# Kernel optimization log

Measured on AMD Instinct MI355X. Metric: run time of the kernel, lower is better.

The kernel has to match this reference:

```python
import jax, jax.numpy as jnp
import numpy as np

FS = 256  # sampling_rate
BANDS = [(0.5, 45.0), (0.5, 4.0), (4.0, 8.0), (8.0, 13.0), (13.0, 30.0), (30.0, 45.0)]
EPS = 1e-8


def _bandpass(sig, lo, hi):
    # FFT-domain brick-wall bandpass, matching bandpass_filter_fft
    T = sig.shape[-1]
    F = jnp.fft.rfft(sig, axis=-1)
    freqs = np.fft.rfftfreq(T, d=1.0 / FS)
    mask = jnp.asarray(((freqs >= lo) & (freqs <= hi)).astype(np.float32))
    return jnp.fft.irfft(F * mask, n=T, axis=-1)


def _phase(sig):
    # Hilbert transform -> instantaneous phase
    T = sig.shape[-1]
    h = np.zeros(T, np.float32)
    if T % 2 == 0:
        h[0] = 1.0; h[T // 2] = 1.0; h[1:T // 2] = 2.0
    else:
        h[0] = 1.0; h[1:(T + 1) // 2] = 2.0
    analytic = jnp.fft.ifft(jnp.fft.fft(sig, axis=-1) * jnp.asarray(h), axis=-1)
    return jnp.angle(analytic)


def _zscore(x):
    # matches torch: (x - mean) / (std_unbiased + 1e-8)
    m = x.mean(-1, keepdims=True)
    s = jnp.std(x, axis=-1, keepdims=True, ddof=1)
    return (x - m) / (s + EPS)


def _band_feats(e1, e2, lo, hi):
    B, C, T = e1.shape
    f1 = _bandpass(e1, lo, hi)
    f2 = _bandpass(e2, lo, hi)
    p1 = f1 ** 2
    p2 = f2 ** 2
    ph1 = _phase(f1)
    ph2 = _phase(f2)

    # PLV = |mean_t exp(i(phi1_i - phi2_j))| -> complex matmul over T
    z1 = jnp.exp(1j * ph1)                       # (B,C,T) complex64
    z2c = jnp.exp(-1j * ph2)
    plv = jnp.abs(jnp.einsum('bit,bjt->bij', z1, z2c)) / T

    # pairwise phase differences (B,C,C,T) -- honors the original full CxC structure
    pd = ph1[:, :, None, :] - ph2[:, None, :, :]
    s = jnp.sign(pd)
    pli = jnp.abs(s.mean(-1))

    # wPLI: power-weighted sign, weights normalized over T per (i,j)
    w = (p1[:, :, None, :] + p2[:, None, :, :]) * 0.5
    wn = w / (w.sum(-1, keepdims=True) + EPS)
    wpli = jnp.abs((s * wn).sum(-1))

    # Coherence: |X_i Y_j*|^2 / (|X_i|^2 |Y_j|^2 + eps), mean over freqs
    X1 = jnp.fft.rfft(f1, axis=-1)
    X2 = jnp.fft.rfft(f2, axis=-1)
    P1 = jnp.abs(X1) ** 2                        # (B,C,F)
    P2 = jnp.abs(X2) ** 2
    pw = P1[:, :, None, :] * P2[:, None, :, :]   # == |pxy|^2 == pxx*pyy
    coh = (pw / (pw + EPS)).mean(-1)

    # Power correlation: z-score over T then matmul / T
    pz1 = _zscore(p1)
    pz2 = _zscore(p2)
    pcorr = jnp.einsum('bit,bjt->bij', pz1, pz2) / T

    # Phase difference magnitude
    phdiff = jnp.abs(pd).mean(-1)

    # Time-domain correlation
    tz1 = _zscore(f1)
    tz2 = _zscore(f2)
    tcorr = jnp.einsum('bit,bjt->bij', tz1, tz2) / T

    # feature order: PLV, PLI, wPLI, Coherence, Power_Corr, Phase_Diff, Time_Corr
    return jnp.stack([plv, pli, wpli, coh, pcorr, phdiff, tcorr], axis=1)  # (B,7,C,C)


def setup_inputs() -> dict:
    key = jax.random.key(0)
    k1, k2 = jax.random.split(key)
    eeg1 = jax.random.normal(k1, (4, 64, 2048), dtype=jnp.float32)
    eeg2 = jax.random.normal(k2, (4, 64, 2048), dtype=jnp.float32)
    return {"eeg1": eeg1, "eeg2": eeg2}


def reference(eeg1, eeg2):
    # feature_type='all' -> all 7 features, 6 bands -> (B, 6, 7, C, C)
    feats = [_band_feats(eeg1, eeg2, lo, hi) for lo, hi in BANDS]
    return jnp.stack(feats, axis=1)
```

## Files before the change

kernel.cpp:

```cpp
#include <hip/hip_runtime.h>
#include <math.h>

__constant__ int c_klo[6] = {4, 4, 32, 64, 104, 240};
__constant__ int c_nk[6]  = {357, 29, 33, 41, 137, 121};

#define PI2_N 0.0030679615757712823f

__global__ __launch_bounds__(256) void k_dft(const float* __restrict__ e1,
                                             const float* __restrict__ e2,
                                             float2* __restrict__ coef,
                                             float* __restrict__ pwr) {
  __shared__ float xs[2048];
  __shared__ float red[4][64][2];
  int sig = blockIdx.x;
  int b = sig >> 7, side = (sig >> 6) & 1, ch = sig & 63;
  int bside = b * 2 + side;
  const float* src = (side ? e2 : e1) + (size_t)(b * 64 + ch) * 2048;
  for (int q = 0; q < 2; ++q) {
    int i4 = q * 256 + threadIdx.x;
    ((float4*)xs)[i4] = ((const float4*)src)[i4];
  }
  __syncthreads();
  int binlane = threadIdx.x & 63, tch = threadIdx.x >> 6;
  int t0 = tch << 9;
  const float* xp = xs + t0;
  for (int rnd = 0; rnd < 6; ++rnd) {
    int kidx = rnd * 64 + binlane;
    int k = kidx + 4;
    float wr, wi, sr, si;
    sincosf(-(float)((k * t0) & 2047) * PI2_N, &wi, &wr);
    sincosf(-(float)k * PI2_N, &si, &sr);
    float are = 0.f, aim = 0.f;
    for (int tt = 0; tt < 512; tt += 4) {
      float4 xv = *(const float4*)(xp + tt);
      float nr, ni;
      are = fmaf(xv.x, wr, are); aim = fmaf(xv.x, wi, aim);
      nr = fmaf(wr, sr, -(wi * si)); ni = fmaf(wr, si, wi * sr); wr = nr; wi = ni;
      are = fmaf(xv.y, wr, are); aim = fmaf(xv.y, wi, aim);
      nr = fmaf(wr, sr, -(wi * si)); ni = fmaf(wr, si, wi * sr); wr = nr; wi = ni;
      are = fmaf(xv.z, wr, are); aim = fmaf(xv.z, wi, aim);
      nr = fmaf(wr, sr, -(wi * si)); ni = fmaf(wr, si, wi * sr); wr = nr; wi = ni;
      are = fmaf(xv.w, wr, are); aim = fmaf(xv.w, wi, aim);
      nr = fmaf(wr, sr, -(wi * si)); ni = fmaf(wr, si, wi * sr); wr = nr; wi = ni;
    }
    red[tch][binlane][0] = are;
    red[tch][binlane][1] = aim;
    __syncthreads();
    if (tch == 0 && kidx < 357) {
      float rr = red[0][binlane][0] + red[1][binlane][0] + red[2][binlane][0] + red[3][binlane][0];
      float ri = red[0][binlane][1] + red[1][binlane][1] + red[2][binlane][1] + red[3][binlane][1];
      int a = (bside * 357 + kidx) * 64 + ch;
      coef[a] = make_float2(rr, ri);
      pwr[a] = rr * rr + ri * ri;
    }
    __syncthreads();
  }
}

__global__ __launch_bounds__(256, 1) void k_analytic(const float2* __restrict__ coef,
                                                     float* __restrict__ fields,
                                                     float* __restrict__ statp4) {
  __shared__ float Fs[65 * 128];
  __shared__ float Ltr[4 * 64 * 65];
  int tchunk = blockIdx.x, bside = blockIdx.y;
  int lane = threadIdx.x & 63;
  int wv = threadIdx.x >> 6;
  int ch0 = wv * 16;
  int t = tchunk * 64 + lane;
  float Rr, Ri;
  sincosf((float)t * PI2_N, &Ri, &Rr);
  float asr[16], asi[16];
#pragma unroll
  for (int c = 0; c < 16; ++c) { asr[c] = 0.f; asi[c] = 0.f; }

  auto emit = [&](int bb, const float (&xr)[16], const float (&xi)[16]) {
#pragma unroll
    for (int c = 0; c < 16; ++c) {
      float re = xr[c] * (1.f / 1024.f);
      float im = xi[c] * (1.f / 1024.f);
      float mag2 = fmaf(re, re, im * im);
      float rinv = mag2 > 0.f ? rsqrtf(mag2) : 0.f;
      float cc = mag2 > 0.f ? re * rinv : 1.f;
      float ss = im * rinv;
      float ph = atan2f(im, re);
      int ca = (ch0 + c) * 65 + lane;
      Ltr[ca] = ph;
      Ltr[4160 + ca] = cc;
      Ltr[8320 + ca] = ss;
      Ltr[12480 + ca] = re;
    }
    __syncthreads();
    size_t pb = (size_t)((bb * 8 + bside) * 4) * 131072 + (size_t)tchunk * 4096;
    for (int f = 0; f < 4; ++f) {
      float* op = fields + pb + (size_t)f * 131072;
      const float* lp = Ltr + f * 4160;
      for (int idx = threadIdx.x; idx < 1024; idx += 256) {
        int tt = idx >> 4;
        int c4 = (idx & 15) * 4;
        float4 v = make_float4(lp[(c4 + 0) * 65 + tt], lp[(c4 + 1) * 65 + tt],
                               lp[(c4 + 2) * 65 + tt], lp[(c4 + 3) * 65 + tt]);
        *(float4*)(op + tt * 64 + c4) = v;
      }
    }
    if (threadIdx.x < 64) {
      const float* lp = Ltr + 12480 + threadIdx.x * 65;
      float s = 0.f;
      for (int tt = 0; tt < 64; ++tt) { float v = lp[tt]; float p = v * v; s = fmaf(p, p, s); }
      statp4[((bb * 8 + bside) * 32 + tchunk) * 64 + threadIdx.x] = s;
    }
    __syncthreads();
  };

  for (int bnd = 1; bnd <= 5; ++bnd) {
    int klo = c_klo[bnd], nk = c_nk[bnd];
    float ar_[16], ai_[16];
#pragma unroll
    for (int c = 0; c < 16; ++c) { ar_[c] = 0.f; ai_[c] = 0.f; }
    float Wr, Wi;
    { int m = (klo * t) & 2047; sincosf((float)m * PI2_N, &Wi, &Wr); }
    for (int c0 = 0; c0 < nk; c0 += 64) {
      int kc = min(64, nk - c0);
      __syncthreads();
      {
        int cbase = (bside * 357 + (klo - 4) + c0) * 64;
        const float4* srcp = (const float4*)(coef + cbase);
        for (int idx = threadIdx.x; idx < kc * 32; idx += 256)
          ((float4*)Fs)[idx] = srcp[idx];
      }
      __syncthreads();
      if (c0 == 0 && bnd >= 2) {
        const float4* Fk = ((const float4*)Fs) + (ch0 >> 1);
#pragma unroll
        for (int q = 0; q < 8; ++q) {
          float4 F = Fk[q];
          asr[2 * q]     = fmaf(-F.x, Wr, asr[2 * q]);     asr[2 * q]     = fmaf( F.y, Wi, asr[2 * q]);
          asi[2 * q]     = fmaf(-F.x, Wi, asi[2 * q]);     asi[2 * q]     = fmaf(-F.y, Wr, asi[2 * q]);
          asr[2 * q + 1] = fmaf(-F.z, Wr, asr[2 * q + 1]); asr[2 * q + 1] = fmaf( F.w, Wi, asr[2 * q + 1]);
          asi[2 * q + 1] = fmaf(-F.z, Wi, asi[2 * q + 1]); asi[2 * q + 1] = fmaf(-F.w, Wr, asi[2 * q + 1]);
        }
      }
      const float4* Fp = ((const float4*)Fs) + (ch0 >> 1);
      float4 Fa[8];
#pragma unroll
      for (int q = 0; q < 8; ++q) Fa[q] = Fp[q];
      for (int kk = 0; kk < kc; ++kk) {
        float4 Fb[8];
        const float4* Fn = Fp + 32;
#pragma unroll
        for (int q = 0; q < 8; ++q) Fb[q] = Fn[q];
#pragma unroll
        for (int q = 0; q < 8; ++q) {
          float4 F = Fa[q];
          ar_[2 * q]     = fmaf(F.x, Wr, ar_[2 * q]);     ar_[2 * q]     = fmaf(-F.y, Wi, ar_[2 * q]);
          ai_[2 * q]     = fmaf(F.x, Wi, ai_[2 * q]);     ai_[2 * q]     = fmaf( F.y, Wr, ai_[2 * q]);
          ar_[2 * q + 1] = fmaf(F.z, Wr, ar_[2 * q + 1]); ar_[2 * q + 1] = fmaf(-F.w, Wi, ar_[2 * q + 1]);
          ai_[2 * q + 1] = fmaf(F.z, Wi, ai_[2 * q + 1]); ai_[2 * q + 1] = fmaf( F.w, Wr, ai_[2 * q + 1]);
        }
        float t0r = Wr * Rr, t1i = Wr * Ri;
        Wr = fmaf(-Wi, Ri, t0r);
        Wi = fmaf(Wi, Rr, t1i);
#pragma unroll
        for (int q = 0; q < 8; ++q) Fa[q] = Fb[q];
        Fp += 32;
      }
    }
#pragma unroll
    for (int c = 0; c < 16; ++c) { asr[c] += ar_[c]; asi[c] += ai_[c]; }
    emit(bnd, ar_, ai_);
  }
  emit(0, asr, asi);
}

__global__ __launch_bounds__(256) void k_statred(const float* __restrict__ statp4,
                                                 const float* __restrict__ pwr,
                                                 float* __restrict__ stats) {
  int gid = blockIdx.x * 256 + threadIdx.x;
  int band = gid >> 9, bsd = (gid >> 6) & 7, ch = gid & 63;
  int klo = c_klo[band], nk = c_nk[band];
  const float* pp = pwr + ((bsd * 357) + (klo - 4)) * 64 + ch;
  float sp = 0.f;
  for (int kk = 0; kk < nk; ++kk) sp += pp[kk * 64];
  sp *= (1.f / 1024.f);
  const float* qp = statp4 + (size_t)((band * 8 + bsd) * 32) * 64 + ch;
  float sq = 0.f;
  for (int tc = 0; tc < 32; ++tc) sq += qp[tc * 64];
  stats[gid * 2] = sp;
  stats[gid * 2 + 1] = sq;
}

__global__ __launch_bounds__(256) void k_pairs(const float* __restrict__ fields,
                                               float* __restrict__ part) {
  __shared__ float li[4 * 16 * 32];
  __shared__ float lj[4 * 16 * 64];
  int ts = blockIdx.x, itile = blockIdx.y, bb = blockIdx.z;
  int band = bb >> 2, b = bb & 3;
  int tid = threadIdx.x;
  int ti = tid >> 4, tj = tid & 15;
  const float* pi = fields + (size_t)((band * 8 + b * 2 + 0) * 4) * 131072;
  const float* pj = fields + (size_t)((band * 8 + b * 2 + 1) * 4) * 131072;
  float aP[2][4], aQ[2][4], aSg[2][4], aS1[2][4], aS2[2][4], aAp[2][4], aPp[2][4], aFf[2][4];
#pragma unroll
  for (int il = 0; il < 2; ++il)
#pragma unroll
    for (int jl = 0; jl < 4; ++jl) {
      aP[il][jl] = 0.f; aQ[il][jl] = 0.f; aSg[il][jl] = 0.f; aS1[il][jl] = 0.f;
      aS2[il][jl] = 0.f; aAp[il][jl] = 0.f; aPp[il][jl] = 0.f; aFf[il][jl] = 0.f;
    }
  int tb = ts * 128;
  for (int sub = 0; sub < 8; ++sub) {
    int t0 = tb + sub * 16;
#pragma unroll
    for (int q = 0; q < 2; ++q) {
      int fl = (q * 256 + tid) * 4;
      int f = fl >> 9, tt = (fl >> 5) & 15, cc = fl & 31;
      *(float4*)&li[fl] = *(const float4*)(pi + (size_t)f * 131072 + (t0 + tt) * 64 + itile * 32 + cc);
    }
#pragma unroll
    for (int q = 0; q < 4; ++q) {
      int fl = (q * 256 + tid) * 4;
      int f = fl >> 10, tt = (fl >> 6) & 15, cc = fl & 63;
      *(float4*)&lj[fl] = *(const float4*)(pj + (size_t)f * 131072 + (t0 + tt) * 64 + cc);
    }
    __syncthreads();
#pragma unroll 2
    for (int tt = 0; tt < 16; ++tt) {
      float2 ph1 = *(const float2*)&li[tt * 32 + ti * 2];
      float2 c1 = *(const float2*)&li[512 + tt * 32 + ti * 2];
      float2 s1 = *(const float2*)&li[1024 + tt * 32 + ti * 2];
      float2 f1 = *(const float2*)&li[1536 + tt * 32 + ti * 2];
      float4 ph2 = *(const float4*)&lj[tt * 64 + tj * 4];
      float4 c2 = *(const float4*)&lj[1024 + tt * 64 + tj * 4];
      float4 s2 = *(const float4*)&lj[2048 + tt * 64 + tj * 4];
      float4 f2 = *(const float4*)&lj[3072 + tt * 64 + tj * 4];
      float ph1a[2] = {ph1.x, ph1.y}, c1a[2] = {c1.x, c1.y}, s1a[2] = {s1.x, s1.y}, f1a[2] = {f1.x, f1.y};
      float ph2a[4] = {ph2.x, ph2.y, ph2.z, ph2.w};
      float c2a[4] = {c2.x, c2.y, c2.z, c2.w};
      float s2a[4] = {s2.x, s2.y, s2.z, s2.w};
      float f2a[4] = {f2.x, f2.y, f2.z, f2.w};
      float p1a[2] = {f1a[0] * f1a[0], f1a[1] * f1a[1]};
      float n1a[2] = {-p1a[0], -p1a[1]};
      float p2a[4] = {f2a[0] * f2a[0], f2a[1] * f2a[1], f2a[2] * f2a[2], f2a[3] * f2a[3]};
      float n2a[4] = {-p2a[0], -p2a[1], -p2a[2], -p2a[3]};
#pragma unroll
      for (int il = 0; il < 2; ++il) {
#pragma unroll
        for (int jl = 0; jl < 4; ++jl) {
          float pd = ph1a[il] - ph2a[jl];
          bool pos = pd > 0.f;
          aSg[il][jl] += pos ? 1.f : -1.f;
          aS1[il][jl] += pos ? p1a[il] : n1a[il];
          aS2[il][jl] += pos ? p2a[jl] : n2a[jl];
          aAp[il][jl] += fabsf(pd);
          aP[il][jl] = fmaf(c1a[il], c2a[jl], aP[il][jl]);
          aP[il][jl] = fmaf(s1a[il], s2a[jl], aP[il][jl]);
          aQ[il][jl] = fmaf(s1a[il], c2a[jl], aQ[il][jl]);
          aQ[il][jl] = fmaf(-c1a[il], s2a[jl], aQ[il][jl]);
          aPp[il][jl] = fmaf(p1a[il], p2a[jl], aPp[il][jl]);
          aFf[il][jl] = fmaf(f1a[il], f2a[jl], aFf[il][jl]);
        }
      }
    }
    __syncthreads();
  }
  int pb = (bb * 16 + ts) * 8;
#pragma unroll
  for (int il = 0; il < 2; ++il) {
    int ro = itile * 2048 + (ti * 2 + il) * 64 + tj * 4;
    *(float4*)&part[(size_t)(pb + 0) * 4096 + ro] = make_float4(aP[il][0], aP[il][1], aP[il][2], aP[il][3]);
    *(float4*)&part[(size_t)(pb + 1) * 4096 + ro] = make_float4(aQ[il][0], aQ[il][1], aQ[il][2], aQ[il][3]);
    *(float4*)&part[(size_t)(pb + 2) * 4096 + ro] = make_float4(aSg[il][0], aSg[il][1], aSg[il][2], aSg[il][3]);
    *(float4*)&part[(size_t)(pb + 3) * 4096 + ro] = make_float4(aS1[il][0], aS1[il][1], aS1[il][2], aS1[il][3]);
    *(float4*)&part[(size_t)(pb + 4) * 4096 + ro] = make_float4(aS2[il][0], aS2[il][1], aS2[il][2], aS2[il][3]);
    *(float4*)&part[(size_t)(pb + 5) * 4096 + ro] = make_float4(aAp[il][0], aAp[il][1], aAp[il][2], aAp[il][3]);
    *(float4*)&part[(size_t)(pb + 6) * 4096 + ro] = make_float4(aPp[il][0], aPp[il][1], aPp[il][2], aPp[il][3]);
    *(float4*)&part[(size_t)(pb + 7) * 4096 + ro] = make_float4(aFf[il][0], aFf[il][1], aFf[il][2], aFf[il][3]);
  }
}

__global__ __launch_bounds__(256) void k_final(const float* __restrict__ part,
                                               const float* __restrict__ stats,
                                               const float* __restrict__ pwr,
                                               float* __restrict__ out) {
  int gid = blockIdx.x * 256 + threadIdx.x;
  int bb = gid >> 12, rem = gid & 4095;
  int band = bb >> 2, b = bb & 3;
  int i = rem >> 6, j = rem & 63;
  float S[8];
#pragma unroll
  for (int a = 0; a < 8; ++a) S[a] = 0.f;
  const float* pp = part + (size_t)bb * 16 * 8 * 4096 + rem;
  for (int ts = 0; ts < 16; ++ts)
#pragma unroll
    for (int a = 0; a < 8; ++a) S[a] += pp[(ts * 8 + a) * 4096];
  const float* st1 = stats + (size_t)((band * 8 + b * 2 + 0) * 64 + i) * 2;
  const float* st2 = stats + (size_t)((band * 8 + b * 2 + 1) * 64 + j) * 2;
  float sp1 = st1[0], sq1 = st1[1];
  float sp2 = st2[0], sq2 = st2[1];
  const float T = 2048.f, Ti = 1.f / 2048.f, Vi = 1.f / 2047.f;
  float plv = sqrtf(S[0] * S[0] + S[1] * S[1]) * Ti;
  float pli = fabsf(S[2]) * Ti;
  float wpli = fabsf(0.5f * (S[3] + S[4])) / (0.5f * (sp1 + sp2) + 1e-8f);
  int kl = c_klo[band] - 4, n = c_nk[band];
  const float* P1 = pwr + ((b * 2 + 0) * 357 + kl) * 64 + i;
  const float* P2 = pwr + ((b * 2 + 1) * 357 + kl) * 64 + j;
  float coh = 0.f;
  for (int kk = 0; kk < n; ++kk) {
    float r = P1[kk * 64] * P2[kk * 64];
    coh += __fdividef(r, r + 1e-8f);
  }
  coh *= (1.f / 1025.f);
  float mp1 = sp1 * Ti, mp2 = sp2 * Ti;
  float sd1 = sqrtf(fmaxf((sq1 - T * mp1 * mp1) * Vi, 0.f));
  float sd2 = sqrtf(fmaxf((sq2 - T * mp2 * mp2) * Vi, 0.f));
  float pcorr = (S[6] - T * mp1 * mp2) / ((sd1 + 1e-8f) * (sd2 + 1e-8f)) * Ti;
  float phd = S[5] * Ti;
  float se1 = sqrtf(sp1 * Vi);
  float se2 = sqrtf(sp2 * Vi);
  float tcorr = S[7] / ((se1 + 1e-8f) * (se2 + 1e-8f)) * Ti;
  size_t ob = (size_t)((b * 6 + band) * 7) * 4096 + rem;
  out[ob] = plv;
  out[ob + 4096] = pli;
  out[ob + 2 * 4096] = wpli;
  out[ob + 3 * 4096] = coh;
  out[ob + 4 * 4096] = pcorr;
  out[ob + 5 * 4096] = phd;
  out[ob + 6 * 4096] = tcorr;
}

extern "C" void kernel_launch(void* const* d_in, const int* in_sizes, int n_in,
                              void* d_out, int out_size, void* d_ws, size_t ws_size,
                              hipStream_t stream) {
  const float* e1 = (const float*)d_in[0];
  const float* e2 = (const float*)d_in[1];
  float* out = (float*)d_out;
  char* ws = (char*)d_ws;
  size_t off = 0;
  auto alloc = [&](size_t bytes) -> void* {
    void* p = ws + off;
    off += (bytes + 255) & ~(size_t)255;
    return p;
  };
  float2* coef = (float2*)alloc((size_t)8 * 357 * 64 * 8);
  float* pwr = (float*)alloc((size_t)8 * 357 * 64 * 4);
  float* fields = (float*)alloc((size_t)6 * 8 * 4 * 2048 * 64 * 4);
  float* statp4 = (float*)alloc((size_t)6 * 8 * 32 * 64 * 4);
  float* stats = (float*)alloc((size_t)6 * 8 * 64 * 2 * 4);
  float* part = (float*)alloc((size_t)24 * 16 * 8 * 4096 * 4);
  (void)in_sizes; (void)n_in; (void)out_size; (void)ws_size;

  hipLaunchKernelGGL(k_dft, dim3(512), dim3(256), 0, stream, e1, e2, coef, pwr);
  hipLaunchKernelGGL(k_analytic, dim3(32, 8), dim3(256), 0, stream, coef, fields, statp4);
  hipLaunchKernelGGL(k_statred, dim3(12), dim3(256), 0, stream, statp4, pwr, stats);
  hipLaunchKernelGGL(k_pairs, dim3(16, 2, 24), dim3(256), 0, stream, fields, part);
  hipLaunchKernelGGL(k_final, dim3(384), dim3(256), 0, stream, part, stats, pwr, out);
}
```

Baseline: 401.8 us.

## Split analytic-signal synthesis across band groups and move phase math into pair kernel

The analytic-signal kernel now runs on three independent frequency splits (bands 1-3, band 4, band 5) per block instead of one serial walk over all bands. It reads coefficients straight from global memory and stores only the real and imaginary parts. A new kernel builds band 0 by summing bands 1-5 and removing the overlapping boundary bins. The pair kernel now computes phase, cos and sin on load, uses full 64x64 tiles with 4x4 register blocking, and accumulates the fourth-power statistics. Time correlation is taken from a Parseval dot product over the DFT coefficients in the final kernel, which drops one accumulator. The aim is more parallelism in the serial synthesis stage and less field memory traffic, at the cost of redundant atan2 work and higher register pressure in the pair kernel.

```diff
diff --git a/kernel.cpp b/kernel.cpp
--- a/kernel.cpp
+++ b/kernel.cpp
@@ -57,241 +57,247 @@
   }
 }
 
-__global__ __launch_bounds__(256, 1) void k_analytic(const float2* __restrict__ coef,
-                                                     float* __restrict__ fields,
-                                                     float* __restrict__ statp4) {
-  __shared__ float Fs[65 * 128];
-  __shared__ float Ltr[4 * 64 * 65];
-  int tchunk = blockIdx.x, bside = blockIdx.y;
+__global__ __launch_bounds__(256) void k_analytic(const float* __restrict__ coef,
+                                                  float* __restrict__ fields) {
+  __shared__ float Lt[2][64][65];
+  int tchunk = blockIdx.x, bside = blockIdx.y, split = blockIdx.z;
   int lane = threadIdx.x & 63;
-  int wv = threadIdx.x >> 6;
-  int ch0 = wv * 16;
+  int ch0 = (threadIdx.x >> 6) << 4;
   int t = tchunk * 64 + lane;
-  float Rr, Ri;
-  sincosf((float)t * PI2_N, &Ri, &Rr);
-  float asr[16], asi[16];
-#pragma unroll
-  for (int c = 0; c < 16; ++c) { asr[c] = 0.f; asi[c] = 0.f; }
-
-  auto emit = [&](int bb, const float (&xr)[16], const float (&xi)[16]) {
+  float Rr, Ri; sincosf((float)t * PI2_N, &Ri, &Rr);
+  int k0 = (split == 0) ? 4 : (split == 1 ? 104 : 240);
+  float Wr, Wi; { int m = (k0 * t) & 2047; sincosf((float)m * PI2_N, &Wi, &Wr); }
+  float ar[16], ai[16];
+#pragma unroll
+  for (int c = 0; c < 16; ++c) { ar[c] = 0.f; ai[c] = 0.f; }
+  const float* cb = coef + (size_t)(bside * 357 + (k0 - 4)) * 128 + ch0 * 2;
+  int kk = 0;
+
+  auto accum = [&](int n) {
+    int e = kk + n;
+#pragma unroll 2
+    for (; kk < e; ++kk) {
+      const float* F = cb + (size_t)kk * 128;
+#pragma unroll
+      for (int q = 0; q < 8; ++q) {
+        float4 Fv = *(const float4*)(F + q * 4);
+        ar[2 * q]     = fmaf(Fv.x, Wr, ar[2 * q]);     ar[2 * q]     = fmaf(-Fv.y, Wi, ar[2 * q]);
+        ai[2 * q]     = fmaf(Fv.x, Wi, ai[2 * q]);     ai[2 * q]     = fmaf( Fv.y, Wr, ai[2 * q]);
+        ar[2 * q + 1] = fmaf(Fv.z, Wr, ar[2 * q + 1]); ar[2 * q + 1] = fmaf(-Fv.w, Wi, ar[2 * q + 1]);
+        ai[2 * q + 1] = fmaf(Fv.z, Wi, ai[2 * q + 1]); ai[2 * q + 1] = fmaf( Fv.w, Wr, ai[2 * q + 1]);
+      }
+      float nr = fmaf(Wr, Rr, -(Wi * Ri));
+      float ni = fmaf(Wr, Ri, Wi * Rr);
+      Wr = nr; Wi = ni;
+    }
+  };
+
+  auto emitBand = [&](int band) {
 #pragma unroll
     for (int c = 0; c < 16; ++c) {
-      float re = xr[c] * (1.f / 1024.f);
-      float im = xi[c] * (1.f / 1024.f);
-      float mag2 = fmaf(re, re, im * im);
-      float rinv = mag2 > 0.f ? rsqrtf(mag2) : 0.f;
-      float cc = mag2 > 0.f ? re * rinv : 1.f;
-      float ss = im * rinv;
-      float ph = atan2f(im, re);
-      int ca = (ch0 + c) * 65 + lane;
-      Ltr[ca] = ph;
-      Ltr[4160 + ca] = cc;
-      Ltr[8320 + ca] = ss;
-      Ltr[12480 + ca] = re;
-    }
-    __syncthreads();
-    size_t pb = (size_t)((bb * 8 + bside) * 4) * 131072 + (size_t)tchunk * 4096;
-    for (int f = 0; f < 4; ++f) {
-      float* op = fields + pb + (size_t)f * 131072;
-      const float* lp = Ltr + f * 4160;
-      for (int idx = threadIdx.x; idx < 1024; idx += 256) {
-        int tt = idx >> 4;
-        int c4 = (idx & 15) * 4;
-        float4 v = make_float4(lp[(c4 + 0) * 65 + tt], lp[(c4 + 1) * 65 + tt],
-                               lp[(c4 + 2) * 65 + tt], lp[(c4 + 3) * 65 + tt]);
-        *(float4*)(op + tt * 64 + c4) = v;
-      }
-    }
-    if (threadIdx.x < 64) {
-      const float* lp = Ltr + 12480 + threadIdx.x * 65;
-      float s = 0.f;
-      for (int tt = 0; tt < 64; ++tt) { float v = lp[tt]; float p = v * v; s = fmaf(p, p, s); }
-      statp4[((bb * 8 + bside) * 32 + tchunk) * 64 + threadIdx.x] = s;
-    }
-    __syncthreads();
+      Lt[0][ch0 + c][lane] = ar[c] * (1.f / 1024.f);
+      Lt[1][ch0 + c][lane] = ai[c] * (1.f / 1024.f);
+    }
+    __syncthreads();
+    size_t base = (size_t)((band * 8 + bside) * 2) * 131072 + (size_t)tchunk * 4096;
+    for (int idx = threadIdx.x; idx < 2048; idx += 256) {
+      int fi = idx >> 10, r = idx & 1023, tt = r >> 4, c4 = (r & 15) * 4;
+      float4 v = make_float4(Lt[fi][c4][tt], Lt[fi][c4 + 1][tt], Lt[fi][c4 + 2][tt], Lt[fi][c4 + 3][tt]);
+      *(float4*)(fields + base + (size_t)fi * 131072 + tt * 64 + c4) = v;
+    }
+    __syncthreads();
+#pragma unroll
+    for (int c = 0; c < 16; ++c) { ar[c] = 0.f; ai[c] = 0.f; }
   };
 
-  for (int bnd = 1; bnd <= 5; ++bnd) {
-    int klo = c_klo[bnd], nk = c_nk[bnd];
-    float ar_[16], ai_[16];
-#pragma unroll
-    for (int c = 0; c < 16; ++c) { ar_[c] = 0.f; ai_[c] = 0.f; }
-    float Wr, Wi;
-    { int m = (klo * t) & 2047; sincosf((float)m * PI2_N, &Wi, &Wr); }
-    for (int c0 = 0; c0 < nk; c0 += 64) {
-      int kc = min(64, nk - c0);
-      __syncthreads();
-      {
-        int cbase = (bside * 357 + (klo - 4) + c0) * 64;
-        const float4* srcp = (const float4*)(coef + cbase);
-        for (int idx = threadIdx.x; idx < kc * 32; idx += 256)
-          ((float4*)Fs)[idx] = srcp[idx];
-      }
-      __syncthreads();
-      if (c0 == 0 && bnd >= 2) {
-        const float4* Fk = ((const float4*)Fs) + (ch0 >> 1);
-#pragma unroll
-        for (int q = 0; q < 8; ++q) {
-          float4 F = Fk[q];
-          asr[2 * q]     = fmaf(-F.x, Wr, asr[2 * q]);     asr[2 * q]     = fmaf( F.y, Wi, asr[2 * q]);
-          asi[2 * q]     = fmaf(-F.x, Wi, asi[2 * q]);     asi[2 * q]     = fmaf(-F.y, Wr, asi[2 * q]);
-          asr[2 * q + 1] = fmaf(-F.z, Wr, asr[2 * q + 1]); asr[2 * q + 1] = fmaf( F.w, Wi, asr[2 * q + 1]);
-          asi[2 * q + 1] = fmaf(-F.z, Wi, asi[2 * q + 1]); asi[2 * q + 1] = fmaf(-F.w, Wr, asi[2 * q + 1]);
-        }
-      }
-      const float4* Fp = ((const float4*)Fs) + (ch0 >> 1);
-      float4 Fa[8];
-#pragma unroll
-      for (int q = 0; q < 8; ++q) Fa[q] = Fp[q];
-      for (int kk = 0; kk < kc; ++kk) {
-        float4 Fb[8];
-        const float4* Fn = Fp + 32;
-#pragma unroll
-        for (int q = 0; q < 8; ++q) Fb[q] = Fn[q];
-#pragma unroll
-        for (int q = 0; q < 8; ++q) {
-          float4 F = Fa[q];
-          ar_[2 * q]     = fmaf(F.x, Wr, ar_[2 * q]);     ar_[2 * q]     = fmaf(-F.y, Wi, ar_[2 * q]);
-          ai_[2 * q]     = fmaf(F.x, Wi, ai_[2 * q]);     ai_[2 * q]     = fmaf( F.y, Wr, ai_[2 * q]);
-          ar_[2 * q + 1] = fmaf(F.z, Wr, ar_[2 * q + 1]); ar_[2 * q + 1] = fmaf(-F.w, Wi, ar_[2 * q + 1]);
-          ai_[2 * q + 1] = fmaf(F.z, Wi, ai_[2 * q + 1]); ai_[2 * q + 1] = fmaf( F.w, Wr, ai_[2 * q + 1]);
-        }
-        float t0r = Wr * Rr, t1i = Wr * Ri;
-        Wr = fmaf(-Wi, Ri, t0r);
-        Wi = fmaf(Wi, Rr, t1i);
-#pragma unroll
-        for (int q = 0; q < 8; ++q) Fa[q] = Fb[q];
-        Fp += 32;
-      }
-    }
-#pragma unroll
-    for (int c = 0; c < 16; ++c) { asr[c] += ar_[c]; asi[c] += ai_[c]; }
-    emit(bnd, ar_, ai_);
-  }
-  emit(0, asr, asi);
-}
-
-__global__ __launch_bounds__(256) void k_statred(const float* __restrict__ statp4,
-                                                 const float* __restrict__ pwr,
-                                                 float* __restrict__ stats) {
-  int gid = blockIdx.x * 256 + threadIdx.x;
-  int band = gid >> 9, bsd = (gid >> 6) & 7, ch = gid & 63;
-  int klo = c_klo[band], nk = c_nk[band];
-  const float* pp = pwr + ((bsd * 357) + (klo - 4)) * 64 + ch;
-  float sp = 0.f;
-  for (int kk = 0; kk < nk; ++kk) sp += pp[kk * 64];
-  sp *= (1.f / 1024.f);
-  const float* qp = statp4 + (size_t)((band * 8 + bsd) * 32) * 64 + ch;
-  float sq = 0.f;
-  for (int tc = 0; tc < 32; ++tc) sq += qp[tc * 64];
-  stats[gid * 2] = sp;
-  stats[gid * 2 + 1] = sq;
-}
-
-__global__ __launch_bounds__(256) void k_pairs(const float* __restrict__ fields,
-                                               float* __restrict__ part) {
-  __shared__ float li[4 * 16 * 32];
-  __shared__ float lj[4 * 16 * 64];
-  int ts = blockIdx.x, itile = blockIdx.y, bb = blockIdx.z;
+  auto stepback = [&]() {
+    float nr = fmaf(Wr, Rr, Wi * Ri);
+    float ni = fmaf(Wi, Rr, -(Wr * Ri));
+    Wr = nr; Wi = ni; kk -= 1;
+  };
+
+  if (split == 0) {
+    accum(29); emitBand(1); stepback();
+    accum(33); emitBand(2); stepback();
+    accum(41); emitBand(3);
+  } else if (split == 1) {
+    accum(137); emitBand(4);
+  } else {
+    accum(121); emitBand(5);
+  }
+}
+
+__global__ __launch_bounds__(256) void k_band0(const float* __restrict__ fields_in,
+                                               const float* __restrict__ coef,
+                                               float* __restrict__ fields) {
+  int idx = blockIdx.x * 256 + threadIdx.x;
+  int ch = idx & 63, t = (idx >> 6) & 2047, bsd = idx >> 17;
+  size_t o = (size_t)t * 64 + ch;
+  float re = 0.f, im = 0.f;
+#pragma unroll
+  for (int b = 1; b <= 5; ++b) {
+    re += fields_in[(size_t)((b * 8 + bsd) * 2 + 0) * 131072 + o];
+    im += fields_in[(size_t)((b * 8 + bsd) * 2 + 1) * 131072 + o];
+  }
+  const int dk[4] = {32, 64, 104, 240};
+#pragma unroll
+  for (int q = 0; q < 4; ++q) {
+    int k = dk[q];
+    const float* F = coef + ((size_t)(bsd * 357 + (k - 4)) * 64 + ch) * 2;
+    float fx = F[0], fy = F[1];
+    float s, c; sincosf((float)((k * t) & 2047) * PI2_N, &s, &c);
+    re -= (fx * c - fy * s) * (1.f / 1024.f);
+    im -= (fx * s + fy * c) * (1.f / 1024.f);
+  }
+  fields[(size_t)(bsd * 2 + 0) * 131072 + o] = re;
+  fields[(size_t)(bsd * 2 + 1) * 131072 + o] = im;
+}
+
+__global__ __launch_bounds__(256, 2) void k_pairs(const float* __restrict__ fields,
+                                                  float* __restrict__ part,
+                                                  float* __restrict__ sqp) {
+  __shared__ float le[2][4][16][64];
+  int ts = blockIdx.x, bb = blockIdx.y;
   int band = bb >> 2, b = bb & 3;
   int tid = threadIdx.x;
   int ti = tid >> 4, tj = tid & 15;
-  const float* pi = fields + (size_t)((band * 8 + b * 2 + 0) * 4) * 131072;
-  const float* pj = fields + (size_t)((band * 8 + b * 2 + 1) * 4) * 131072;
-  float aP[2][4], aQ[2][4], aSg[2][4], aS1[2][4], aS2[2][4], aAp[2][4], aPp[2][4], aFf[2][4];
-#pragma unroll
-  for (int il = 0; il < 2; ++il)
-#pragma unroll
-    for (int jl = 0; jl < 4; ++jl) {
-      aP[il][jl] = 0.f; aQ[il][jl] = 0.f; aSg[il][jl] = 0.f; aS1[il][jl] = 0.f;
-      aS2[il][jl] = 0.f; aAp[il][jl] = 0.f; aPp[il][jl] = 0.f; aFf[il][jl] = 0.f;
-    }
+  const float* bi = fields + (size_t)((band * 8 + b * 2 + 0) * 2) * 131072;
+  const float* bj = fields + (size_t)((band * 8 + b * 2 + 1) * 2) * 131072;
+  float acc[7][4][4];
+#pragma unroll
+  for (int a = 0; a < 7; ++a)
+#pragma unroll
+    for (int il = 0; il < 4; ++il)
+#pragma unroll
+      for (int jl = 0; jl < 4; ++jl) acc[a][il][jl] = 0.f;
+  float sqa = 0.f;
+  int lside = tid >> 7, lr = tid & 127, ltt = lr >> 3, lc8 = (lr & 7) * 8;
+  const float* lbase = lside ? bj : bi;
+  int sside = (tid >> 6) & 1, sch = tid & 63, shalf = tid >> 7;
   int tb = ts * 128;
   for (int sub = 0; sub < 8; ++sub) {
     int t0 = tb + sub * 16;
-#pragma unroll
-    for (int q = 0; q < 2; ++q) {
-      int fl = (q * 256 + tid) * 4;
-      int f = fl >> 9, tt = (fl >> 5) & 15, cc = fl & 31;
-      *(float4*)&li[fl] = *(const float4*)(pi + (size_t)f * 131072 + (t0 + tt) * 64 + itile * 32 + cc);
-    }
-#pragma unroll
-    for (int q = 0; q < 4; ++q) {
-      int fl = (q * 256 + tid) * 4;
-      int f = fl >> 10, tt = (fl >> 6) & 15, cc = fl & 63;
-      *(float4*)&lj[fl] = *(const float4*)(pj + (size_t)f * 131072 + (t0 + tt) * 64 + cc);
-    }
-    __syncthreads();
+    {
+      const float* rp = lbase + (size_t)(t0 + ltt) * 64 + lc8;
+      float4 reA = *(const float4*)rp;
+      float4 reB = *(const float4*)(rp + 4);
+      float4 imA = *(const float4*)(rp + 131072);
+      float4 imB = *(const float4*)(rp + 131072 + 4);
+      float re8[8] = {reA.x, reA.y, reA.z, reA.w, reB.x, reB.y, reB.z, reB.w};
+      float im8[8] = {imA.x, imA.y, imA.z, imA.w, imB.x, imB.y, imB.z, imB.w};
+#pragma unroll
+      for (int e = 0; e < 8; ++e) {
+        float re = re8[e], im = im8[e];
+        float mag2 = fmaf(re, re, im * im);
+        float rinv = mag2 > 0.f ? rsqrtf(mag2) : 0.f;
+        float cc = mag2 > 0.f ? re * rinv : 1.f;
+        float ss = im * rinv;
+        float ph = atan2f(im, re);
+        le[lside][0][ltt][lc8 + e] = ph;
+        le[lside][1][ltt][lc8 + e] = cc;
+        le[lside][2][ltt][lc8 + e] = ss;
+        le[lside][3][ltt][lc8 + e] = re;
+      }
+    }
+    __syncthreads();
+#pragma unroll
+    for (int u = 0; u < 8; ++u) {
+      float v = le[sside][3][shalf * 8 + u][sch];
+      float p = v * v;
+      sqa = fmaf(p, p, sqa);
+    }
 #pragma unroll 2
     for (int tt = 0; tt < 16; ++tt) {
-      float2 ph1 = *(const float2*)&li[tt * 32 + ti * 2];
-      float2 c1 = *(const float2*)&li[512 + tt * 32 + ti * 2];
-      float2 s1 = *(const float2*)&li[1024 + tt * 32 + ti * 2];
-      float2 f1 = *(const float2*)&li[1536 + tt * 32 + ti * 2];
-      float4 ph2 = *(const float4*)&lj[tt * 64 + tj * 4];
-      float4 c2 = *(const float4*)&lj[1024 + tt * 64 + tj * 4];
-      float4 s2 = *(const float4*)&lj[2048 + tt * 64 + tj * 4];
-      float4 f2 = *(const float4*)&lj[3072 + tt * 64 + tj * 4];
-      float ph1a[2] = {ph1.x, ph1.y}, c1a[2] = {c1.x, c1.y}, s1a[2] = {s1.x, s1.y}, f1a[2] = {f1.x, f1.y};
-      float ph2a[4] = {ph2.x, ph2.y, ph2.z, ph2.w};
-      float c2a[4] = {c2.x, c2.y, c2.z, c2.w};
-      float s2a[4] = {s2.x, s2.y, s2.z, s2.w};
-      float f2a[4] = {f2.x, f2.y, f2.z, f2.w};
-      float p1a[2] = {f1a[0] * f1a[0], f1a[1] * f1a[1]};
-      float n1a[2] = {-p1a[0], -p1a[1]};
+      float4 vph1 = *(const float4*)&le[0][0][tt][ti * 4];
+      float4 vc1 = *(const float4*)&le[0][1][tt][ti * 4];
+      float4 vs1 = *(const float4*)&le[0][2][tt][ti * 4];
+      float4 vf1 = *(const float4*)&le[0][3][tt][ti * 4];
+      float4 vph2 = *(const float4*)&le[1][0][tt][tj * 4];
+      float4 vc2 = *(const float4*)&le[1][1][tt][tj * 4];
+      float4 vs2 = *(const float4*)&le[1][2][tt][tj * 4];
+      float4 vf2 = *(const float4*)&le[1][3][tt][tj * 4];
+      float ph1a[4] = {vph1.x, vph1.y, vph1.z, vph1.w};
+      float c1a[4] = {vc1.x, vc1.y, vc1.z, vc1.w};
+      float s1a[4] = {vs1.x, vs1.y, vs1.z, vs1.w};
+      float f1a[4] = {vf1.x, vf1.y, vf1.z, vf1.w};
+      float ph2a[4] = {vph2.x, vph2.y, vph2.z, vph2.w};
+      float c2a[4] = {vc2.x, vc2.y, vc2.z, vc2.w};
+      float s2a[4] = {vs2.x, vs2.y, vs2.z, vs2.w};
+      float f2a[4] = {vf2.x, vf2.y, vf2.z, vf2.w};
+      float p1a[4] = {f1a[0] * f1a[0], f1a[1] * f1a[1], f1a[2] * f1a[2], f1a[3] * f1a[3]};
       float p2a[4] = {f2a[0] * f2a[0], f2a[1] * f2a[1], f2a[2] * f2a[2], f2a[3] * f2a[3]};
-      float n2a[4] = {-p2a[0], -p2a[1], -p2a[2], -p2a[3]};
-#pragma unroll
-      for (int il = 0; il < 2; ++il) {
+#pragma unroll
+      for (int il = 0; il < 4; ++il) {
 #pragma unroll
         for (int jl = 0; jl < 4; ++jl) {
           float pd = ph1a[il] - ph2a[jl];
-          bool pos = pd > 0.f;
-          aSg[il][jl] += pos ? 1.f : -1.f;
-          aS1[il][jl] += pos ? p1a[il] : n1a[il];
-          aS2[il][jl] += pos ? p2a[jl] : n2a[jl];
-          aAp[il][jl] += fabsf(pd);
-          aP[il][jl] = fmaf(c1a[il], c2a[jl], aP[il][jl]);
-          aP[il][jl] = fmaf(s1a[il], s2a[jl], aP[il][jl]);
-          aQ[il][jl] = fmaf(s1a[il], c2a[jl], aQ[il][jl]);
-          aQ[il][jl] = fmaf(-c1a[il], s2a[jl], aQ[il][jl]);
-          aPp[il][jl] = fmaf(p1a[il], p2a[jl], aPp[il][jl]);
-          aFf[il][jl] = fmaf(f1a[il], f2a[jl], aFf[il][jl]);
+          float sg = pd > 0.f ? 1.f : -1.f;
+          acc[2][il][jl] += sg;
+          acc[3][il][jl] = fmaf(sg, p1a[il], acc[3][il][jl]);
+          acc[4][il][jl] = fmaf(sg, p2a[jl], acc[4][il][jl]);
+          acc[5][il][jl] += fabsf(pd);
+          acc[0][il][jl] = fmaf(c1a[il], c2a[jl], acc[0][il][jl]);
+          acc[0][il][jl] = fmaf(s1a[il], s2a[jl], acc[0][il][jl]);
+          acc[1][il][jl] = fmaf(s1a[il], c2a[jl], acc[1][il][jl]);
+          acc[1][il][jl] = fmaf(-c1a[il], s2a[jl], acc[1][il][jl]);
+          acc[6][il][jl] = fmaf(p1a[il], p2a[jl], acc[6][il][jl]);
         }
       }
     }
     __syncthreads();
   }
-  int pb = (bb * 16 + ts) * 8;
-#pragma unroll
-  for (int il = 0; il < 2; ++il) {
-    int ro = itile * 2048 + (ti * 2 + il) * 64 + tj * 4;
-    *(float4*)&part[(size_t)(pb + 0) * 4096 + ro] = make_float4(aP[il][0], aP[il][1], aP[il][2], aP[il][3]);
-    *(float4*)&part[(size_t)(pb + 1) * 4096 + ro] = make_float4(aQ[il][0], aQ[il][1], aQ[il][2], aQ[il][3]);
-    *(float4*)&part[(size_t)(pb + 2) * 4096 + ro] = make_float4(aSg[il][0], aSg[il][1], aSg[il][2], aSg[il][3]);
-    *(float4*)&part[(size_t)(pb + 3) * 4096 + ro] = make_float4(aS1[il][0], aS1[il][1], aS1[il][2], aS1[il][3]);
-    *(float4*)&part[(size_t)(pb + 4) * 4096 + ro] = make_float4(aS2[il][0], aS2[il][1], aS2[il][2], aS2[il][3]);
-    *(float4*)&part[(size_t)(pb + 5) * 4096 + ro] = make_float4(aAp[il][0], aAp[il][1], aAp[il][2], aAp[il][3]);
-    *(float4*)&part[(size_t)(pb + 6) * 4096 + ro] = make_float4(aPp[il][0], aPp[il][1], aPp[il][2], aPp[il][3]);
-    *(float4*)&part[(size_t)(pb + 7) * 4096 + ro] = make_float4(aFf[il][0], aFf[il][1], aFf[il][2], aFf[il][3]);
-  }
+  int pb = (bb * 16 + ts) * 7;
+#pragma unroll
+  for (int a = 0; a < 7; ++a)
+#pragma unroll
+    for (int il = 0; il < 4; ++il) {
+      int ro = (ti * 4 + il) * 64 + tj * 4;
+      *(float4*)&part[(size_t)(pb + a) * 4096 + ro] =
+          make_float4(acc[a][il][0], acc[a][il][1], acc[a][il][2], acc[a][il][3]);
+    }
+  ((float*)le)[tid] = sqa;
+  __syncthreads();
+  if (tid < 128) {
+    sqp[(size_t)(bb * 16 + ts) * 128 + tid] = ((float*)le)[tid] + ((float*)le)[tid + 128];
+  }
+}
+
+__global__ __launch_bounds__(256) void k_stats(const float* __restrict__ pwr,
+                                               const float* __restrict__ sqp,
+                                               float* __restrict__ stats) {
+  int gid = blockIdx.x * 256 + threadIdx.x;
+  int band = gid >> 9, bsd = (gid >> 6) & 7, ch = gid & 63;
+  int b = bsd >> 1, side = bsd & 1;
+  int kl = c_klo[band] - 4, nk = c_nk[band];
+  const float* pp = pwr + (size_t)(bsd * 357 + kl) * 64 + ch;
+  float sp = 0.f;
+  for (int kkq = 0; kkq < nk; ++kkq) sp += pp[kkq * 64];
+  sp *= (1.f / 1024.f);
+  int bb = band * 4 + b;
+  const float* qp = sqp + (size_t)(bb * 16) * 128 + side * 64 + ch;
+  float sq = 0.f;
+#pragma unroll 4
+  for (int tsq = 0; tsq < 16; ++tsq) sq += qp[tsq * 128];
+  stats[gid * 2] = sp;
+  stats[gid * 2 + 1] = sq;
 }
 
 __global__ __launch_bounds__(256) void k_final(const float* __restrict__ part,
                                                const float* __restrict__ stats,
                                                const float* __restrict__ pwr,
+                                               const float* __restrict__ coef,
                                                float* __restrict__ out) {
   int gid = blockIdx.x * 256 + threadIdx.x;
   int bb = gid >> 12, rem = gid & 4095;
   int band = bb >> 2, b = bb & 3;
   int i = rem >> 6, j = rem & 63;
-  float S[8];
-#pragma unroll
-  for (int a = 0; a < 8; ++a) S[a] = 0.f;
-  const float* pp = part + (size_t)bb * 16 * 8 * 4096 + rem;
+  float S[7];
+#pragma unroll
+  for (int a = 0; a < 7; ++a) S[a] = 0.f;
+  const float* pp = part + (size_t)bb * 16 * 7 * 4096 + rem;
   for (int ts = 0; ts < 16; ++ts)
 #pragma unroll
-    for (int a = 0; a < 8; ++a) S[a] += pp[(ts * 8 + a) * 4096];
+    for (int a = 0; a < 7; ++a) S[a] += pp[(ts * 7 + a) * 4096];
   const float* st1 = stats + (size_t)((band * 8 + b * 2 + 0) * 64 + i) * 2;
   const float* st2 = stats + (size_t)((band * 8 + b * 2 + 1) * 64 + j) * 2;
   float sp1 = st1[0], sq1 = st1[1];
@@ -301,12 +307,17 @@
   float pli = fabsf(S[2]) * Ti;
   float wpli = fabsf(0.5f * (S[3] + S[4])) / (0.5f * (sp1 + sp2) + 1e-8f);
   int kl = c_klo[band] - 4, n = c_nk[band];
-  const float* P1 = pwr + ((b * 2 + 0) * 357 + kl) * 64 + i;
-  const float* P2 = pwr + ((b * 2 + 1) * 357 + kl) * 64 + j;
-  float coh = 0.f;
-  for (int kk = 0; kk < n; ++kk) {
-    float r = P1[kk * 64] * P2[kk * 64];
+  const float* P1 = pwr + (size_t)((b * 2 + 0) * 357 + kl) * 64 + i;
+  const float* P2 = pwr + (size_t)((b * 2 + 1) * 357 + kl) * 64 + j;
+  const float* C1 = coef + ((size_t)((b * 2 + 0) * 357 + kl) * 64 + i) * 2;
+  const float* C2 = coef + ((size_t)((b * 2 + 1) * 357 + kl) * 64 + j) * 2;
+  float coh = 0.f, cross = 0.f;
+  for (int kkq = 0; kkq < n; ++kkq) {
+    float r = P1[kkq * 64] * P2[kkq * 64];
     coh += __fdividef(r, r + 1e-8f);
+    float2 a = *(const float2*)(C1 + kkq * 128);
+    float2 c = *(const float2*)(C2 + kkq * 128);
+    cross = fmaf(a.x, c.x, fmaf(a.y, c.y, cross));
   }
   coh *= (1.f / 1025.f);
   float mp1 = sp1 * Ti, mp2 = sp2 * Ti;
@@ -316,7 +327,7 @@
   float phd = S[5] * Ti;
   float se1 = sqrtf(sp1 * Vi);
   float se2 = sqrtf(sp2 * Vi);
-  float tcorr = S[7] / ((se1 + 1e-8f) * (se2 + 1e-8f)) * Ti;
+  float tcorr = (cross * (1.f / 1024.f)) / ((se1 + 1e-8f) * (se2 + 1e-8f)) * Ti;
   size_t ob = (size_t)((b * 6 + band) * 7) * 4096 + rem;
   out[ob] = plv;
   out[ob + 4096] = pli;
@@ -342,15 +353,16 @@
   };
   float2* coef = (float2*)alloc((size_t)8 * 357 * 64 * 8);
   float* pwr = (float*)alloc((size_t)8 * 357 * 64 * 4);
-  float* fields = (float*)alloc((size_t)6 * 8 * 4 * 2048 * 64 * 4);
-  float* statp4 = (float*)alloc((size_t)6 * 8 * 32 * 64 * 4);
+  float* fields = (float*)alloc((size_t)6 * 8 * 2 * 131072 * 4);
+  float* sqp = (float*)alloc((size_t)24 * 16 * 128 * 4);
   float* stats = (float*)alloc((size_t)6 * 8 * 64 * 2 * 4);
-  float* part = (float*)alloc((size_t)24 * 16 * 8 * 4096 * 4);
+  float* part = (float*)alloc((size_t)24 * 16 * 7 * 4096 * 4);
   (void)in_sizes; (void)n_in; (void)out_size; (void)ws_size;
 
   hipLaunchKernelGGL(k_dft, dim3(512), dim3(256), 0, stream, e1, e2, coef, pwr);
-  hipLaunchKernelGGL(k_analytic, dim3(32, 8), dim3(256), 0, stream, coef, fields, statp4);
-  hipLaunchKernelGGL(k_statred, dim3(12), dim3(256), 0, stream, statp4, pwr, stats);
-  hipLaunchKernelGGL(k_pairs, dim3(16, 2, 24), dim3(256), 0, stream, fields, part);
-  hipLaunchKernelGGL(k_final, dim3(384), dim3(256), 0, stream, part, stats, pwr, out);
-}
+  hipLaunchKernelGGL(k_analytic, dim3(32, 8, 3), dim3(256), 0, stream, (const float*)coef, fields);
+  hipLaunchKernelGGL(k_band0, dim3(4096), dim3(256), 0, stream, fields, (const float*)coef, fields);
+  hipLaunchKernelGGL(k_pairs, dim3(16, 24), dim3(256), 0, stream, fields, part, sqp);
+  hipLaunchKernelGGL(k_stats, dim3(12), dim3(256), 0, stream, pwr, sqp, stats);
+  hipLaunchKernelGGL(k_final, dim3(384), dim3(256), 0, stream, part, stats, pwr, (const float*)coef, out);
+}
```

Result: slower. 413.7 us (+3.0%).
